# Optimization experiments

Measured on AMD Instinct MI355X. Metric: run time of the kernel, lower is better.

The kernel has to match this reference:

```python
import jax, jax.numpy as jnp
import numpy as np

B, D, E, K = 32768, 512, 64, 4
NCTX = 16
H = (NCTX // 2 - 1) * 768  # 5376: per-expert context block, (n_ctx/2 - 1) rows of ctx_dim=768
NOISE_EPS = 1e-2
LOSS_COEF = 1e-2


def setup_inputs() -> dict:
    key = jax.random.key(0)
    ks = jax.random.split(key, 5)
    x = jax.random.normal(ks[0], (B, D), jnp.float32)
    w_gate = jax.random.normal(ks[1], (D, E), jnp.float32) * 0.02
    w_noise = jax.random.normal(ks[2], (D, E), jnp.float32) * 0.02
    noise = jax.random.normal(ks[3], (B, E), jnp.float32)
    ctx_c = jax.random.normal(ks[4], (E, H), jnp.float32) * 0.02
    return {"x": x, "w_gate": w_gate, "w_noise": w_noise, "noise": noise, "ctx_c": ctx_c}


def _cv_squared(v, eps=1e-10):
    # coefficient-of-variation squared: var / mean^2
    return jnp.var(v) / (jnp.mean(v) ** 2 + eps)


def _normal_cdf(z):
    return 0.5 * (1.0 + jax.lax.erf(z * (1.0 / np.sqrt(2.0))))


def reference(x, w_gate, w_noise, noise, ctx_c):
    # ---- noisy top-k gating (Shazeer sparsely-gated MoE) ----
    clean_logits = x @ w_gate                                    # [B, E]
    noise_stddev = jax.nn.softplus(x @ w_noise) + NOISE_EPS      # [B, E]
    noisy_logits = clean_logits + noise * noise_stddev           # [B, E]

    top_logits, top_idx = jax.lax.top_k(noisy_logits, K + 1)     # [B, K+1]
    top_k_logits = top_logits[:, :K]
    top_k_idx = top_idx[:, :K]
    top_k_gates = jax.nn.softmax(top_k_logits, axis=-1)          # [B, K]

    rows = jnp.arange(B)[:, None]
    gates = jnp.zeros((B, E), x.dtype).at[rows, top_k_idx].set(top_k_gates)  # sparse -> dense scatter

    # ---- load-balancing aux loss ----
    importance = gates.sum(axis=0)                               # [E]
    thr_in = top_logits[:, K][:, None]                           # (K+1)-th largest noisy logit
    thr_out = top_logits[:, K - 1][:, None]                      # K-th largest noisy logit
    is_in = noisy_logits > thr_in
    prob_in = _normal_cdf((clean_logits - thr_in) / noise_stddev)
    prob_out = _normal_cdf((clean_logits - thr_out) / noise_stddev)
    load = jnp.where(is_in, prob_in, prob_out).sum(axis=0)       # [E]
    aux_loss = (_cv_squared(importance) + _cv_squared(load)) * LOSS_COEF

    # ---- weighted combine of per-expert context vectors (as in LPromptLearner) ----
    out = jnp.einsum('be,eh->bh', gates, ctx_c)                  # [B, H]
    return out, aux_loss
```

## Files before the change

kernel.cpp:

```cpp
#include <hip/hip_runtime.h>
#include <math.h>

#define B_ 32768
#define D_ 512
#define E_ 64
#define H_ 5376
#define H4_ (H_ / 4)
#define HC_ 128
#define NCH_ (H_ / HC_)

typedef float f32x4 __attribute__((ext_vector_type(4)));
typedef _Float16 f16x8 __attribute__((ext_vector_type(8)));
typedef unsigned int u32x4 __attribute__((ext_vector_type(4)));

__device__ __forceinline__ unsigned short f16bits(_Float16 h) {
    union { _Float16 h; unsigned short u; } c; c.h = h; return c.u;
}

__global__ __launch_bounds__(256) void prep_kernel(
    const float* __restrict__ wgate, const float* __restrict__ wnoise,
    _Float16* __restrict__ wt0, _Float16* __restrict__ wt1)
{
    int e = blockIdx.x;
    const float* src = (e < E_) ? (wgate + e) : (wnoise + (e - E_));
    for (int k = threadIdx.x; k < D_; k += 256) {
        float v = src[(size_t)k * E_] * 1024.0f;
        _Float16 h0 = (_Float16)v;
        _Float16 h1 = (_Float16)(v - (float)h0);
        wt0[(size_t)e * D_ + k] = h0;
        wt1[(size_t)e * D_ + k] = h1;
    }
}

#define TOP5_STEP(TV, TI)                                              \
    {                                                                  \
        double bm = v0; int bj = 0;                                    \
        if (v1 > bm) { bm = v1; bj = 1; }                              \
        if (v2 > bm) { bm = v2; bj = 2; }                              \
        if (v3 > bm) { bm = v3; bj = 3; }                              \
        int be = bj * 16 + le;                                         \
        _Pragma("unroll")                                              \
        for (int off = 1; off < 16; off <<= 1) {                       \
            double om = __shfl_xor(bm, off, 64);                       \
            int    oe = __shfl_xor(be, off, 64);                       \
            if (om > bm || (om == bm && oe < be)) { bm = om; be = oe; }\
        }                                                              \
        TV = bm; TI = be;                                              \
        bool wn = ((be & 15) == le); int sl = be >> 4;                 \
        v0 = (wn && sl == 0) ? -1.0e300 : v0;                          \
        v1 = (wn && sl == 1) ? -1.0e300 : v1;                          \
        v2 = (wn && sl == 2) ? -1.0e300 : v2;                          \
        v3 = (wn && sl == 3) ? -1.0e300 : v3;                          \
    }

__global__ __launch_bounds__(256) void gate_kernel(
    const float* __restrict__ x,
    const _Float16* __restrict__ wt0,
    const _Float16* __restrict__ wt1,
    const float* __restrict__ noise,
    unsigned int* __restrict__ o_idx,
    float4* __restrict__ o_g,
    float* __restrict__ g_imp,
    float* __restrict__ g_load)
{
    __shared__ __align__(16) _Float16 x0s[64 * 128];
    __shared__ __align__(16) _Float16 x1s[64 * 128];
    __shared__ float s_imp[E_];
    __shared__ float s_load[E_];

    const int t  = threadIdx.x;
    const int w  = t >> 6;
    const int l  = t & 63;
    const int le = l & 15;
    const int g  = l >> 4;
    const int b0 = blockIdx.x * 64;
    const int arow = w * 16 + le;

    if (t < E_) { s_imp[t] = 0.0f; s_load[t] = 0.0f; }

    f32x4 accAC[8], accB[8];
#pragma unroll
    for (int n = 0; n < 8; ++n) {
        accAC[n] = (f32x4){0.f, 0.f, 0.f, 0.f};
        accB[n]  = (f32x4){0.f, 0.f, 0.f, 0.f};
    }

    for (int q = 0; q < 4; ++q) {
        __syncthreads();
#pragma unroll
        for (int i = 0; i < 4; ++i) {
            int id  = t + 256 * i;
            int row = id >> 4;
            int c   = id & 15;
            const float* src = x + (size_t)(b0 + row) * D_ + q * 128 + c * 8;
            float4 v0 = *(const float4*)src;
            float4 v1 = *(const float4*)(src + 4);
            float vv[8] = {v0.x, v0.y, v0.z, v0.w, v1.x, v1.y, v1.z, v1.w};
            unsigned int hw[4], lw[4];
#pragma unroll
            for (int p = 0; p < 4; ++p) {
                float va = vv[2*p] * 16.0f, vb = vv[2*p+1] * 16.0f;
                _Float16 a0 = (_Float16)va, b0f = (_Float16)vb;
                _Float16 a1 = (_Float16)((va - (float)a0) * 4096.0f);
                _Float16 b1 = (_Float16)((vb - (float)b0f) * 4096.0f);
                hw[p] = (unsigned)f16bits(a0) | ((unsigned)f16bits(b0f) << 16);
                lw[p] = (unsigned)f16bits(a1) | ((unsigned)f16bits(b1) << 16);
            }
            int addr = (row * 256 + c * 16) ^ ((row & 7) << 4);
            *(u32x4*)((char*)x0s + addr) = (u32x4){hw[0], hw[1], hw[2], hw[3]};
            *(u32x4*)((char*)x1s + addr) = (u32x4){lw[0], lw[1], lw[2], lw[3]};
        }
        __syncthreads();
#pragma unroll
        for (int s = 0; s < 4; ++s) {
            int aoff = (arow * 256 + s * 64 + g * 16) ^ ((arow & 7) << 4);
            f16x8 a0 = *(const f16x8*)((const char*)x0s + aoff);
            f16x8 a1 = *(const f16x8*)((const char*)x1s + aoff);
            int ks = q * 4 + s;
#pragma unroll
            for (int n = 0; n < 8; ++n) {
                size_t boff = (size_t)(n * 16 + le) * D_ + ks * 32 + g * 8;
                f16x8 b0 = *(const f16x8*)(wt0 + boff);
                f16x8 b1 = *(const f16x8*)(wt1 + boff);
                accAC[n] = __builtin_amdgcn_mfma_f32_16x16x32_f16(a0, b0, accAC[n], 0, 0, 0);
                accAC[n] = __builtin_amdgcn_mfma_f32_16x16x32_f16(a0, b1, accAC[n], 0, 0, 0);
                accB[n]  = __builtin_amdgcn_mfma_f32_16x16x32_f16(a1, b0, accB[n],  0, 0, 0);
            }
        }
    }

    const double UNSCALE = 1.0 / 16384.0;
    const double RESC    = 1.0 / 4096.0;
    float loadacc[4] = {0.f, 0.f, 0.f, 0.f};
#pragma unroll
    for (int r = 0; r < 4; ++r) {
        int li = w * 16 + g * 4 + r;
        int b  = b0 + li;
        double cl[4], ny[4];
        float  sdf[4];
#pragma unroll
        for (int n = 0; n < 4; ++n) {
            cl[n] = ((double)accAC[n][r] + (double)accB[n][r] * RESC) * UNSCALE;
            float z = (float)(((double)accAC[n+4][r] + (double)accB[n+4][r] * RESC) * UNSCALE);
            float sp = (z > 20.0f) ? z : log1pf(expf(z));
            sdf[n] = sp + 0.01f;
            float nz = noise[(size_t)b * E_ + le + 16 * n];
            ny[n] = cl[n] + (double)(nz * sdf[n]);
        }
        double v0 = ny[0], v1 = ny[1], v2 = ny[2], v3 = ny[3];
        double tv0, tv1, tv2, tv3, tv4;
        int    ti0, ti1, ti2, ti3, ti4;
        TOP5_STEP(tv0, ti0)
        TOP5_STEP(tv1, ti1)
        TOP5_STEP(tv2, ti2)
        TOP5_STEP(tv3, ti3)
        TOP5_STEP(tv4, ti4)
        float e1 = expf((float)(tv1 - tv0)),
              e2 = expf((float)(tv2 - tv0)),
              e3 = expf((float)(tv3 - tv0));
        float inv = 1.0f / (1.0f + e1 + e2 + e3);
        float g0 = inv, g1 = e1 * inv, g2 = e2 * inv, g3 = e3 * inv;
        if (le == 0) {
            o_idx[b] = (unsigned)ti0 | ((unsigned)ti1 << 8) |
                       ((unsigned)ti2 << 16) | ((unsigned)ti3 << 24);
            float4 gv; gv.x = g0; gv.y = g1; gv.z = g2; gv.w = g3;
            o_g[b] = gv;
            atomicAdd(&s_imp[ti0], g0);
            atomicAdd(&s_imp[ti1], g1);
            atomicAdd(&s_imp[ti2], g2);
            atomicAdd(&s_imp[ti3], g3);
        }
        double thr_out = tv3;
        double thr_in  = tv4;
#pragma unroll
        for (int n = 0; n < 4; ++n) {
            double thr = (ny[n] > thr_in) ? thr_in : thr_out;
            float  zz  = (float)(cl[n] - thr) / sdf[n];
            loadacc[n] += 0.5f * (1.0f + erff(zz * 0.70710678118654752f));
        }
    }
#pragma unroll
    for (int n = 0; n < 4; ++n) atomicAdd(&s_load[16 * n + le], loadacc[n]);
    __syncthreads();
    if (t < E_) {
        atomicAdd(&g_imp[t],  s_imp[t]);
        atomicAdd(&g_load[t], s_load[t]);
    }
}

__global__ __launch_bounds__(256) void dispatch_kernel(
    const float* __restrict__ ctx,
    const unsigned int* __restrict__ o_idx,
    const float4* __restrict__ o_g,
    float* __restrict__ out)
{
    __shared__ f32x4 cs[E_ * (HC_ / 4)];

    const int t  = threadIdx.x;
    const int h0 = blockIdx.x * HC_;
    const int tb = blockIdx.y * 64;

#pragma unroll
    for (int i = 0; i < 8; ++i) {
        int idx = t + 256 * i;
        int e = idx >> 5, c = idx & 31;
        cs[idx] = *(const f32x4*)&ctx[(size_t)e * H_ + h0 + c * 4];
    }
    __syncthreads();

    const int tok = t >> 5;
    const int c   = t & 31;
#pragma unroll
    for (int s = 0; s < 8; ++s) {
        int b = tb + s * 8 + tok;
        unsigned pk = o_idx[b];
        float4 g = o_g[b];
        f32x4 r = g.x * cs[((pk      ) & 255u) * 32 + c]
                + g.y * cs[((pk >>  8) & 255u) * 32 + c]
                + g.z * cs[((pk >> 16) & 255u) * 32 + c]
                + g.w * cs[( pk >> 24         ) * 32 + c];
        __builtin_nontemporal_store(r, (f32x4*)&out[(size_t)b * H_ + h0 + c * 4]);
    }
}

__global__ void loss_kernel(const float* __restrict__ g_imp,
                            const float* __restrict__ g_load,
                            float* __restrict__ out)
{
    int e = threadIdx.x;
    double vi = (double)g_imp[e];
    double vl = (double)g_load[e];
    double si = vi, sl = vl;
#pragma unroll
    for (int off = 1; off < 64; off <<= 1) {
        si += __shfl_xor(si, off, 64);
        sl += __shfl_xor(sl, off, 64);
    }
    double mi = si / 64.0, ml = sl / 64.0;
    double di = vi - mi, dl = vl - ml;
    double qi = di * di, ql = dl * dl;
#pragma unroll
    for (int off = 1; off < 64; off <<= 1) {
        qi += __shfl_xor(qi, off, 64);
        ql += __shfl_xor(ql, off, 64);
    }
    double vari = qi / 64.0, varl = ql / 64.0;
    double cv2i = vari / (mi * mi + 1e-10);
    double cv2l = varl / (ml * ml + 1e-10);
    if (e == 0) out[(size_t)B_ * H_] = (float)((cv2i + cv2l) * 0.01);
}

extern "C" void kernel_launch(void* const* d_in, const int* in_sizes, int n_in,
                              void* d_out, int out_size, void* d_ws, size_t ws_size,
                              hipStream_t stream)
{
    const float* x      = (const float*)d_in[0];
    const float* wgate  = (const float*)d_in[1];
    const float* wnoise = (const float*)d_in[2];
    const float* noise  = (const float*)d_in[3];
    const float* ctx    = (const float*)d_in[4];
    float* out    = (float*)d_out;
    float* g_imp  = (float*)d_ws;
    float* g_load = g_imp + E_;
    _Float16* wt0 = (_Float16*)(g_load + E_);
    _Float16* wt1 = wt0 + 128 * D_;
    unsigned int* o_idx = (unsigned int*)(wt1 + 128 * D_);
    float4* o_g = (float4*)(o_idx + B_);

    (void)hipMemsetAsync(d_ws, 0, 2 * E_ * sizeof(float), stream);
    prep_kernel<<<128, 256, 0, stream>>>(wgate, wnoise, wt0, wt1);
    gate_kernel<<<B_ / 64, 256, 0, stream>>>(x, wt0, wt1, noise,
                                             o_idx, o_g, g_imp, g_load);
    dispatch_kernel<<<dim3(NCH_, B_ / 64), 256, 0, stream>>>(ctx, o_idx, o_g, out);
    loss_kernel<<<1, 64, 0, stream>>>(g_imp, g_load, out);
}
```

Measured before the change: 237.5 us.

## Double-buffer x tiles in gate kernel to overlap global loads with MFMA

Turns the x staging buffers in LDS into two buffers. The next 128-column chunk of x is loaded into registers before the MFMA loop runs on the current chunk, then converted and written to the other buffer afterwards. This hides global load latency behind matrix math and drops one barrier per iteration. In exchange it doubles the LDS footprint to 64KB and keeps 8 float4 registers live across the MFMA loop, which may reduce occupancy.

```diff
diff --git a/kernel.cpp b/kernel.cpp
--- a/kernel.cpp
+++ b/kernel.cpp
@@ -53,6 +53,39 @@
         v3 = (wn && sl == 3) ? -1.0e300 : v3;                          \
     }
 
+#define ISSUE_LOADS(Q)                                                         \
+    _Pragma("unroll")                                                          \
+    for (int i = 0; i < 4; ++i) {                                              \
+        int id  = t + 256 * i;                                                 \
+        const float* src = x + (size_t)(b0 + (id >> 4)) * D_ + (Q) * 128 +     \
+                           (id & 15) * 8;                                      \
+        ra[2 * i]     = *(const float4*)src;                                   \
+        ra[2 * i + 1] = *(const float4*)(src + 4);                             \
+    }
+
+#define CONVERT_WRITE(BUF)                                                     \
+    _Pragma("unroll")                                                          \
+    for (int i = 0; i < 4; ++i) {                                              \
+        int id  = t + 256 * i;                                                 \
+        int row = id >> 4;                                                     \
+        int c   = id & 15;                                                     \
+        float vv[8] = {ra[2*i].x, ra[2*i].y, ra[2*i].z, ra[2*i].w,             \
+                       ra[2*i+1].x, ra[2*i+1].y, ra[2*i+1].z, ra[2*i+1].w};    \
+        unsigned int hw[4], lw[4];                                             \
+        _Pragma("unroll")                                                      \
+        for (int p = 0; p < 4; ++p) {                                          \
+            float va = vv[2*p] * 16.0f, vb = vv[2*p+1] * 16.0f;                \
+            _Float16 a0 = (_Float16)va, b0f = (_Float16)vb;                    \
+            _Float16 a1 = (_Float16)((va - (float)a0) * 4096.0f);              \
+            _Float16 b1 = (_Float16)((vb - (float)b0f) * 4096.0f);             \
+            hw[p] = (unsigned)f16bits(a0) | ((unsigned)f16bits(b0f) << 16);    \
+            lw[p] = (unsigned)f16bits(a1) | ((unsigned)f16bits(b1) << 16);     \
+        }                                                                      \
+        int addr = (row * 256 + c * 16) ^ ((row & 7) << 4);                    \
+        *(u32x4*)((char*)x0s[BUF] + addr) = (u32x4){hw[0], hw[1], hw[2], hw[3]};\
+        *(u32x4*)((char*)x1s[BUF] + addr) = (u32x4){lw[0], lw[1], lw[2], lw[3]};\
+    }
+
 __global__ __launch_bounds__(256) void gate_kernel(
     const float* __restrict__ x,
     const _Float16* __restrict__ wt0,
@@ -63,8 +96,8 @@
     float* __restrict__ g_imp,
     float* __restrict__ g_load)
 {
-    __shared__ __align__(16) _Float16 x0s[64 * 128];
-    __shared__ __align__(16) _Float16 x1s[64 * 128];
+    __shared__ __align__(16) _Float16 x0s[2][64 * 128];
+    __shared__ __align__(16) _Float16 x1s[2][64 * 128];
     __shared__ float s_imp[E_];
     __shared__ float s_load[E_];
 
@@ -85,37 +118,19 @@
         accB[n]  = (f32x4){0.f, 0.f, 0.f, 0.f};
     }
 
+    float4 ra[8];
+    ISSUE_LOADS(0)
+    CONVERT_WRITE(0)
+
+#pragma unroll
     for (int q = 0; q < 4; ++q) {
-        __syncthreads();
-#pragma unroll
-        for (int i = 0; i < 4; ++i) {
-            int id  = t + 256 * i;
-            int row = id >> 4;
-            int c   = id & 15;
-            const float* src = x + (size_t)(b0 + row) * D_ + q * 128 + c * 8;
-            float4 v0 = *(const float4*)src;
-            float4 v1 = *(const float4*)(src + 4);
-            float vv[8] = {v0.x, v0.y, v0.z, v0.w, v1.x, v1.y, v1.z, v1.w};
-            unsigned int hw[4], lw[4];
-#pragma unroll
-            for (int p = 0; p < 4; ++p) {
-                float va = vv[2*p] * 16.0f, vb = vv[2*p+1] * 16.0f;
-                _Float16 a0 = (_Float16)va, b0f = (_Float16)vb;
-                _Float16 a1 = (_Float16)((va - (float)a0) * 4096.0f);
-                _Float16 b1 = (_Float16)((vb - (float)b0f) * 4096.0f);
-                hw[p] = (unsigned)f16bits(a0) | ((unsigned)f16bits(b0f) << 16);
-                lw[p] = (unsigned)f16bits(a1) | ((unsigned)f16bits(b1) << 16);
-            }
-            int addr = (row * 256 + c * 16) ^ ((row & 7) << 4);
-            *(u32x4*)((char*)x0s + addr) = (u32x4){hw[0], hw[1], hw[2], hw[3]};
-            *(u32x4*)((char*)x1s + addr) = (u32x4){lw[0], lw[1], lw[2], lw[3]};
-        }
+        if (q < 3) ISSUE_LOADS(q + 1)
         __syncthreads();
 #pragma unroll
         for (int s = 0; s < 4; ++s) {
             int aoff = (arow * 256 + s * 64 + g * 16) ^ ((arow & 7) << 4);
-            f16x8 a0 = *(const f16x8*)((const char*)x0s + aoff);
-            f16x8 a1 = *(const f16x8*)((const char*)x1s + aoff);
+            f16x8 a0 = *(const f16x8*)((const char*)x0s[q & 1] + aoff);
+            f16x8 a1 = *(const f16x8*)((const char*)x1s[q & 1] + aoff);
             int ks = q * 4 + s;
 #pragma unroll
             for (int n = 0; n < 8; ++n) {
@@ -127,6 +142,7 @@
                 accB[n]  = __builtin_amdgcn_mfma_f32_16x16x32_f16(a1, b0, accB[n],  0, 0, 0);
             }
         }
+        if (q < 3) CONVERT_WRITE((q + 1) & 1)
     }
 
     const double UNSCALE = 1.0 / 16384.0;
```

New measurement: 232.7 us. 1.02x faster.

## Load gate activations directly to registers and pre-swizzle weights into MFMA fragment order

Applied to the files above, without the earlier changes.

The gate GEMM no longer stages x through shared memory. Each lane now loads its own A-fragment straight from global memory and splits it into hi/lo fp16 in registers. The prep kernel writes the fp16 weight splits in an MFMA-fragment-major layout, so each B-fragment load is a contiguous per-lane 16-byte read. This removes the LDS traffic and the per-quarter barriers, at the cost of global loads that are less coalesced across a row and redundant conversion work.

```diff
diff --git a/kernel.cpp b/kernel.cpp
--- a/kernel.cpp
+++ b/kernel.cpp
@@ -11,7 +11,6 @@
 
 typedef float f32x4 __attribute__((ext_vector_type(4)));
 typedef _Float16 f16x8 __attribute__((ext_vector_type(8)));
-typedef unsigned int u32x4 __attribute__((ext_vector_type(4)));
 
 __device__ __forceinline__ unsigned short f16bits(_Float16 h) {
     union { _Float16 h; unsigned short u; } c; c.h = h; return c.u;
@@ -22,13 +21,16 @@
     _Float16* __restrict__ wt0, _Float16* __restrict__ wt1)
 {
     int e = blockIdx.x;
+    int n  = e >> 4, le = e & 15;
     const float* src = (e < E_) ? (wgate + e) : (wnoise + (e - E_));
     for (int k = threadIdx.x; k < D_; k += 256) {
         float v = src[(size_t)k * E_] * 1024.0f;
         _Float16 h0 = (_Float16)v;
         _Float16 h1 = (_Float16)(v - (float)h0);
-        wt0[(size_t)e * D_ + k] = h0;
-        wt1[(size_t)e * D_ + k] = h1;
+        int ks = k >> 5, g = (k & 31) >> 3, j = k & 7;
+        size_t idx = ((size_t)(ks * 8 + n) * 64 + g * 16 + le) * 8 + j;
+        wt0[idx] = h0;
+        wt1[idx] = h1;
     }
 }
 
@@ -63,8 +65,6 @@
     float* __restrict__ g_imp,
     float* __restrict__ g_load)
 {
-    __shared__ __align__(16) _Float16 x0s[64 * 128];
-    __shared__ __align__(16) _Float16 x1s[64 * 128];
     __shared__ float s_imp[E_];
     __shared__ float s_load[E_];
 
@@ -74,9 +74,9 @@
     const int le = l & 15;
     const int g  = l >> 4;
     const int b0 = blockIdx.x * 64;
-    const int arow = w * 16 + le;
 
     if (t < E_) { s_imp[t] = 0.0f; s_load[t] = 0.0f; }
+    __syncthreads();
 
     f32x4 accAC[8], accB[8];
 #pragma unroll
@@ -85,47 +85,29 @@
         accB[n]  = (f32x4){0.f, 0.f, 0.f, 0.f};
     }
 
-    for (int q = 0; q < 4; ++q) {
-        __syncthreads();
-#pragma unroll
-        for (int i = 0; i < 4; ++i) {
-            int id  = t + 256 * i;
-            int row = id >> 4;
-            int c   = id & 15;
-            const float* src = x + (size_t)(b0 + row) * D_ + q * 128 + c * 8;
-            float4 v0 = *(const float4*)src;
-            float4 v1 = *(const float4*)(src + 4);
-            float vv[8] = {v0.x, v0.y, v0.z, v0.w, v1.x, v1.y, v1.z, v1.w};
-            unsigned int hw[4], lw[4];
-#pragma unroll
-            for (int p = 0; p < 4; ++p) {
-                float va = vv[2*p] * 16.0f, vb = vv[2*p+1] * 16.0f;
-                _Float16 a0 = (_Float16)va, b0f = (_Float16)vb;
-                _Float16 a1 = (_Float16)((va - (float)a0) * 4096.0f);
-                _Float16 b1 = (_Float16)((vb - (float)b0f) * 4096.0f);
-                hw[p] = (unsigned)f16bits(a0) | ((unsigned)f16bits(b0f) << 16);
-                lw[p] = (unsigned)f16bits(a1) | ((unsigned)f16bits(b1) << 16);
-            }
-            int addr = (row * 256 + c * 16) ^ ((row & 7) << 4);
-            *(u32x4*)((char*)x0s + addr) = (u32x4){hw[0], hw[1], hw[2], hw[3]};
-            *(u32x4*)((char*)x1s + addr) = (u32x4){lw[0], lw[1], lw[2], lw[3]};
-        }
-        __syncthreads();
-#pragma unroll
-        for (int s = 0; s < 4; ++s) {
-            int aoff = (arow * 256 + s * 64 + g * 16) ^ ((arow & 7) << 4);
-            f16x8 a0 = *(const f16x8*)((const char*)x0s + aoff);
-            f16x8 a1 = *(const f16x8*)((const char*)x1s + aoff);
-            int ks = q * 4 + s;
-#pragma unroll
-            for (int n = 0; n < 8; ++n) {
-                size_t boff = (size_t)(n * 16 + le) * D_ + ks * 32 + g * 8;
-                f16x8 b0 = *(const f16x8*)(wt0 + boff);
-                f16x8 b1 = *(const f16x8*)(wt1 + boff);
-                accAC[n] = __builtin_amdgcn_mfma_f32_16x16x32_f16(a0, b0, accAC[n], 0, 0, 0);
-                accAC[n] = __builtin_amdgcn_mfma_f32_16x16x32_f16(a0, b1, accAC[n], 0, 0, 0);
-                accB[n]  = __builtin_amdgcn_mfma_f32_16x16x32_f16(a1, b0, accB[n],  0, 0, 0);
-            }
+    const float* abase = x + (size_t)(b0 + w * 16 + le) * D_ + g * 8;
+
+#pragma unroll 4
+    for (int ks = 0; ks < 16; ++ks) {
+        float4 va = *(const float4*)(abase + ks * 32);
+        float4 vb = *(const float4*)(abase + ks * 32 + 4);
+        float vv[8] = {va.x, va.y, va.z, va.w, vb.x, vb.y, vb.z, vb.w};
+        f16x8 a0, a1;
+#pragma unroll
+        for (int j = 0; j < 8; ++j) {
+            float vs = vv[j] * 16.0f;
+            _Float16 h = (_Float16)vs;
+            a0[j] = h;
+            a1[j] = (_Float16)((vs - (float)h) * 4096.0f);
+        }
+#pragma unroll
+        for (int n = 0; n < 8; ++n) {
+            size_t boff = ((size_t)(ks * 8 + n) * 64 + l) * 8;
+            f16x8 b0f = *(const f16x8*)(wt0 + boff);
+            f16x8 b1f = *(const f16x8*)(wt1 + boff);
+            accAC[n] = __builtin_amdgcn_mfma_f32_16x16x32_f16(a0, b0f, accAC[n], 0, 0, 0);
+            accAC[n] = __builtin_amdgcn_mfma_f32_16x16x32_f16(a0, b1f, accAC[n], 0, 0, 0);
+            accB[n]  = __builtin_amdgcn_mfma_f32_16x16x32_f16(a1, b0f, accB[n],  0, 0, 0);
         }
     }
 
```

After: 199.0 us. 1.19x faster.
